# Optimization experiments

Measured on AMD Instinct MI355X. Metric: run time of the kernel, lower is better.

Reference implementation:

```python
import jax, jax.numpy as jnp
import numpy as np

B, M, D, H, K, V = 4, 2048, 1024, 16, 64, 64

def setup_inputs() -> dict:
    key = jax.random.key(0)
    ks = jax.random.split(key, 5)
    return {
        "x": jax.random.normal(ks[0], (B, M, D), dtype=jnp.float32),
        "P_q": jax.random.normal(ks[1], (H, D, K), dtype=jnp.float32) * 0.02,
        "P_k": jax.random.normal(ks[2], (H, D, K), dtype=jnp.float32) * 0.02,
        "P_v": jax.random.normal(ks[3], (H, D, V), dtype=jnp.float32) * 0.02,
        "P_o": jax.random.normal(ks[4], (H, D, V), dtype=jnp.float32) * 0.02,
    }

def reference(x, P_q, P_k, P_v, P_o):
    # QKV projections: [b,m,d] x [h,d,k] -> [b,h,m,k]
    Q = jnp.einsum('bmd,hdk->bhmk', x, P_q)
    Kt = jnp.einsum('bmd,hdk->bhmk', x, P_k)
    Vt = jnp.einsum('bmd,hdv->bhmv', x, P_v)
    scale = 1.0 / jnp.sqrt(jnp.asarray(K, dtype=x.dtype))
    logits = jnp.einsum('bhmk,bhnk->bhmn', Q, Kt) * scale  # [b,h,m,m]
    m = logits.shape[-1]
    causal = jnp.tril(jnp.ones((m, m), dtype=bool))  # allow j <= i
    logits = jnp.where(causal[None, None], logits, jnp.asarray(-jnp.inf, dtype=logits.dtype))
    weights = jax.nn.softmax(logits, axis=-1)
    o = jnp.einsum('bhmn,bhnv->bhmv', weights, Vt)
    y = jnp.einsum('bhmv,hdv->bmd', o, P_o)
    return y
```

## Files before the change

kernel.cpp:

```cpp
#include <hip/hip_runtime.h>
#include <hip/hip_bf16.h>

#define B_  4
#define M_  2048
#define D_  1024
#define H_  16

typedef __attribute__((ext_vector_type(8)))  short bf16x8;
typedef __attribute__((ext_vector_type(4)))  float f32x4;
typedef __attribute__((ext_vector_type(16))) float f32x16;
typedef __attribute__((ext_vector_type(4)))  unsigned short u16x4;
typedef __attribute__((ext_vector_type(2)))  unsigned int uint2v;

#define MFMA16(a, b, c) __builtin_amdgcn_mfma_f32_16x16x32_bf16((a), (b), (c), 0, 0, 0)
#define MFMA32(a, b, c) __builtin_amdgcn_mfma_f32_32x32x16_bf16((a), (b), (c), 0, 0, 0)

#define QSCALE 0.18033688011112042f

__device__ __forceinline__ unsigned short f2b(float f) {
  union { float f; unsigned u; } v; v.f = f;
  unsigned r = v.u + 0x7FFF + ((v.u >> 16) & 1);
  return (unsigned short)(r >> 16);
}

__device__ __forceinline__ unsigned cvtpk(float lo, float hi) {
  unsigned r;
  asm("v_cvt_pk_bf16_f32 %0, %1, %2" : "=v"(r) : "v"(lo), "v"(hi));
  return r;
}

__device__ __forceinline__ int swzb(int byte) {
  return byte ^ (((byte >> 7) & 7) << 4);
}

#define SWZ256(L) ((L) ^ ((((L) >> 8) & 15) << 4))

#define GLOAD16(gsrc, ldst)                                                     \
  __builtin_amdgcn_global_load_lds(                                             \
      (const __attribute__((address_space(1))) void*)(gsrc),                    \
      (__attribute__((address_space(3))) void*)(ldst), 16, 0, 0)

__global__ __launch_bounds__(256) void convert_x_kernel(
    const float* __restrict__ x, short* __restrict__ xb) {
  const size_t i = ((size_t)blockIdx.x * 256 + threadIdx.x) * 8;
  float4 a = *(const float4*)(x + i);
  float4 b = *(const float4*)(x + i + 4);
  bf16x8 o;
  o[0] = (short)f2b(a.x); o[1] = (short)f2b(a.y); o[2] = (short)f2b(a.z); o[3] = (short)f2b(a.w);
  o[4] = (short)f2b(b.x); o[5] = (short)f2b(b.y); o[6] = (short)f2b(b.z); o[7] = (short)f2b(b.w);
  *(bf16x8*)(xb + i) = o;
}

__global__ __launch_bounds__(256) void convert_w_kernel(
    const float* __restrict__ Pq, const float* __restrict__ Pk,
    const float* __restrict__ Pv, short* __restrict__ Wt) {
  const int idx = blockIdx.x * 256 + threadIdx.x;
  const int n = idx >> 8, d0 = (idx & 255) * 4;
  const int which = n >> 10, h = (n >> 6) & 15, kc = n & 63;
  const float* P = (which == 0) ? Pq : (which == 1) ? Pk : Pv;
  const float* p = P + ((size_t)h * D_ + d0) * 64 + kc;
  u16x4 o;
  o[0] = f2b(p[0]); o[1] = f2b(p[64]); o[2] = f2b(p[128]); o[3] = f2b(p[192]);
  *(u16x4*)(Wt + (size_t)n * D_ + d0) = o;
}

__global__ __launch_bounds__(256) void convert_wo_kernel(
    const float* __restrict__ Po, short* __restrict__ Wo) {
  const int idx = blockIdx.x * 256 + threadIdx.x;
  const int d = idx >> 8, hv0 = (idx & 255) * 4;
  const int h = hv0 >> 6, v = hv0 & 63;
  float4 a = *(const float4*)(Po + ((size_t)h * D_ + d) * 64 + v);
  u16x4 o;
  o[0] = f2b(a.x); o[1] = f2b(a.y); o[2] = f2b(a.z); o[3] = f2b(a.w);
  *(u16x4*)(Wo + (size_t)d * 1024 + hv0) = o;
}

__global__ __launch_bounds__(256) void qkv_gemm_kernel(
    const short* __restrict__ xb, const short* __restrict__ Wt,
    short* __restrict__ Qw, short* __restrict__ Kw, short* __restrict__ Vt) {
  __shared__ short As[128 * 64];
  __shared__ short Bs[128 * 64];
  int bid = blockIdx.x;
  bid = (bid & 7) * 192 + (bid >> 3);
  const int mt = bid & 63, nt = bid >> 6;
  const int m0 = mt * 128, n0 = nt * 128;
  const int t = threadIdx.x, lane = t & 63, w = t >> 6;
  const int wr = (w >> 1) * 64, wc = (w & 1) * 64;
  const int lrow = lane & 15, lgrp = lane >> 4;

  f32x4 acc[4][4] = {};
  const char* Agc = (const char*)xb + (size_t)m0 * D_ * 2;
  const char* Bgc = (const char*)Wt + (size_t)n0 * D_ * 2;

  for (int d0 = 0; d0 < D_; d0 += 64) {
    __syncthreads();
#pragma unroll
    for (int i = 0; i < 4; ++i) {
      const int L = i * 4096 + t * 16;
      const int row = L >> 7;
      const int cb = (L & 127) ^ ((row & 7) << 4);
      GLOAD16(Agc + ((size_t)row * D_ + d0) * 2 + cb, (char*)As + i * 4096 + w * 1024);
      GLOAD16(Bgc + ((size_t)row * D_ + d0) * 2 + cb, (char*)Bs + i * 4096 + w * 1024);
    }
    __syncthreads();
#pragma unroll
    for (int ks = 0; ks < 2; ++ks) {
      bf16x8 a[4], b[4];
      const int cb = ks * 64 + lgrp * 16;
#pragma unroll
      for (int f = 0; f < 4; ++f) {
        a[f] = *(const bf16x8*)((const char*)As + swzb((wr + f * 16 + lrow) * 128 + cb));
        b[f] = *(const bf16x8*)((const char*)Bs + swzb((wc + f * 16 + lrow) * 128 + cb));
      }
#pragma unroll
      for (int mf = 0; mf < 4; ++mf)
#pragma unroll
        for (int nf = 0; nf < 4; ++nf)
          acc[mf][nf] = MFMA16(a[mf], b[nf], acc[mf][nf]);
    }
  }

#pragma unroll
  for (int nf = 0; nf < 4; ++nf) {
    const int n = n0 + wc + nf * 16 + lrow;
    const int which = n >> 10, h = (n >> 6) & 15, kc = n & 63;
#pragma unroll
    for (int mf = 0; mf < 4; ++mf) {
      const int row0 = m0 + wr + mf * 16 + lgrp * 4;
      const int b = row0 >> 11, mm = row0 & 2047;
      const int bh = b * 16 + h;
      if (which == 2) {
        u16x4 o;
        o[0] = f2b(acc[mf][nf][0]); o[1] = f2b(acc[mf][nf][1]);
        o[2] = f2b(acc[mf][nf][2]); o[3] = f2b(acc[mf][nf][3]);
        *(u16x4*)(Vt + ((size_t)bh * 64 + kc) * M_ + mm) = o;
      } else {
        short* outp = (which == 0 ? Qw : Kw) + ((size_t)bh * M_ + mm) * 64 + kc;
        const float scale = (which == 0) ? QSCALE : 1.0f;
#pragma unroll
        for (int r = 0; r < 4; ++r)
          outp[(size_t)r * 64] = (short)f2b(acc[mf][nf][r] * scale);
      }
    }
  }
}

__device__ __forceinline__ void softmax_chunk(
    f32x16& s0, f32x16& s1, f32x16& o0, f32x16& o1,
    float& mrun, float& lrun, bf16x8 (&pf)[4])
{
  float tm[16];
#pragma unroll
  for (int r = 0; r < 16; ++r) tm[r] = fmaxf(s0[r], s1[r]);
#pragma unroll
  for (int st = 8; st > 0; st >>= 1)
#pragma unroll
    for (int r = 0; r < 8; ++r)
      if (r < st) tm[r] = fmaxf(tm[r], tm[r + st]);
  uint2v pm = __builtin_amdgcn_permlane32_swap(
      __float_as_uint(tm[0]), __float_as_uint(tm[0]), false, false);
  const float mtile = fmaxf(__uint_as_float(pm[0]), __uint_as_float(pm[1]));

  if (!__all(mtile <= mrun + 8.0f)) {
    const float mnew = fmaxf(mrun, mtile);
    const float alpha = __builtin_amdgcn_exp2f(mrun - mnew);
    mrun = mnew;
    lrun *= alpha;
    o0 *= alpha;
    o1 *= alpha;
  }
#pragma unroll
  for (int r = 0; r < 16; ++r) {
    s0[r] = __builtin_amdgcn_exp2f(s0[r] - mrun);
    s1[r] = __builtin_amdgcn_exp2f(s1[r] - mrun);
  }
#pragma unroll
  for (int c = 0; c < 4; ++c) {
    const f32x16& sv = (c < 2) ? s0 : s1;
    const int rb = (c & 1) * 8;
    unsigned a0 = cvtpk(sv[rb + 0], sv[rb + 1]);
    unsigned a1 = cvtpk(sv[rb + 2], sv[rb + 3]);
    unsigned b0 = cvtpk(sv[rb + 4], sv[rb + 5]);
    unsigned b1 = cvtpk(sv[rb + 6], sv[rb + 7]);
    uint2v t0 = __builtin_amdgcn_permlane32_swap(a0, b0, false, false);
    uint2v t1 = __builtin_amdgcn_permlane32_swap(a1, b1, false, false);
    union { unsigned u[4]; bf16x8 v; } pk;
    pk.u[0] = t0[0]; pk.u[1] = t1[0]; pk.u[2] = t0[1]; pk.u[3] = t1[1];
    pf[c] = pk.v;
  }
}

__global__ __launch_bounds__(256) void attn_kernel(
    const short* __restrict__ Qw, const short* __restrict__ Kw,
    const short* __restrict__ Vt, short* __restrict__ O2) {
  __shared__ short Ks[2][64 * 64];
  __shared__ short Vs[2][64 * 64];

  const int bid = blockIdx.x;
  const int chunk = 15 - (bid >> 6);
  const int bh = bid & 63;
  const int q0 = chunk * 128;

  const int t = threadIdx.x, lane = t & 63, w = t >> 6;
  const int l31 = lane & 31, hi = lane >> 5;
  const int qw0 = q0 + w * 32;
  const int qabs = qw0 + l31;

  bf16x8 qfrag[4];
#pragma unroll
  for (int kc = 0; kc < 4; ++kc)
    qfrag[kc] = *(const bf16x8*)(Qw + ((size_t)bh * M_ + qabs) * 64 + kc * 16 + hi * 8);

  f32x16 o0 = {}, o1 = {};
  float mrun = -3.0e38f, lrun = 0.f;

  const char* Kg = (const char*)Kw + (size_t)bh * M_ * 128;
  const char* Vg = (const char*)Vt + (size_t)bh * 64 * M_ * 2;

  auto stage = [&](int bi, int j0_) {
#pragma unroll
    for (int i = 0; i < 2; ++i) {
      const int L  = i * 4096 + t * 16;
      const int Ls = SWZ256(L);
      const int row = Ls >> 7, col = Ls & 127;
      GLOAD16(Kg + (size_t)(j0_ + row) * 128 + col, (char*)Ks[bi] + i * 4096 + w * 1024);
      GLOAD16(Vg + (size_t)row * (M_ * 2) + (size_t)j0_ * 2 + col, (char*)Vs[bi] + i * 4096 + w * 1024);
    }
  };

  const int nt = (q0 + 128) >> 6;
  stage(0, 0);

  bf16x8 ones;
#pragma unroll
  for (int e = 0; e < 8; ++e) ones[e] = (short)0x3F80;

  for (int tt = 0; tt < nt; ++tt) {
    const int j0 = tt << 6;
    const int cur = tt & 1;
    __builtin_amdgcn_s_barrier();
    if (tt + 1 < nt) {
      stage(cur ^ 1, j0 + 64);
      asm volatile("s_waitcnt vmcnt(4)" ::: "memory");
    } else {
      asm volatile("s_waitcnt vmcnt(0)" ::: "memory");
    }
    __builtin_amdgcn_s_barrier();
    if (j0 >= qw0 + 32) continue;

    const char* Kc = (const char*)Ks[cur];
    const char* Vc = (const char*)Vs[cur];

    f32x16 s0 = {}, s1 = {};
    __builtin_amdgcn_s_setprio(1);
#pragma unroll
    for (int kc = 0; kc < 4; ++kc) {
      bf16x8 kf0 = *(const bf16x8*)(Kc + SWZ256(l31 * 128 + kc * 32 + hi * 16));
      s0 = MFMA32(kf0, qfrag[kc], s0);
      bf16x8 kf1 = *(const bf16x8*)(Kc + SWZ256((32 + l31) * 128 + kc * 32 + hi * 16));
      s1 = MFMA32(kf1, qfrag[kc], s1);
    }
    __builtin_amdgcn_s_setprio(0);

    if (j0 + 64 > qw0) {
#pragma unroll
      for (int r = 0; r < 16; ++r) {
        const int k0 = j0 + (r & 3) + 8 * (r >> 2) + 4 * hi;
        if (k0 > qabs)      s0[r] = -3.0e38f;
        if (k0 + 32 > qabs) s1[r] = -3.0e38f;
      }
    }

    bf16x8 pf[4];
    softmax_chunk(s0, s1, o0, o1, mrun, lrun, pf);

    f32x16 lacc = {};
    __builtin_amdgcn_s_setprio(1);
#pragma unroll
    for (int c = 0; c < 4; ++c) {
      bf16x8 vf0 = *(const bf16x8*)(Vc + SWZ256(l31 * 128 + c * 32 + hi * 16));
      o0 = MFMA32(vf0, pf[c], o0);
      bf16x8 vf1 = *(const bf16x8*)(Vc + SWZ256((32 + l31) * 128 + c * 32 + hi * 16));
      o1 = MFMA32(vf1, pf[c], o1);
      lacc = MFMA32(ones, pf[c], lacc);
    }
    __builtin_amdgcn_s_setprio(0);
    lrun += lacc[0];
  }

  const int b = bh >> 4, h = bh & 15;
  const float inv = 1.0f / lrun;
  short* orow = O2 + ((size_t)b * M_ + qabs) * 1024 + h * 64;
#pragma unroll
  for (int vb = 0; vb < 2; ++vb) {
    const f32x16& o = vb ? o1 : o0;
#pragma unroll
    for (int g = 0; g < 4; ++g) {
      const int vbase = vb * 32 + 8 * g + 4 * hi;
      u16x4 pkt;
      pkt[0] = f2b(o[g * 4 + 0] * inv);
      pkt[1] = f2b(o[g * 4 + 1] * inv);
      pkt[2] = f2b(o[g * 4 + 2] * inv);
      pkt[3] = f2b(o[g * 4 + 3] * inv);
      *(u16x4*)(orow + vbase) = pkt;
    }
  }
}

__global__ __launch_bounds__(256) void out_gemm_kernel(
    const short* __restrict__ O2, const short* __restrict__ Wo,
    float* __restrict__ y) {
  __shared__ short As[128 * 64];
  __shared__ short Bs[128 * 64];
  int bid = blockIdx.x;
  bid = (bid & 7) * 64 + (bid >> 3);
  const int mt = bid & 63, nt = bid >> 6;
  const int m0 = mt * 128, n0 = nt * 128;
  const int t = threadIdx.x, lane = t & 63, w = t >> 6;
  const int wr = (w >> 1) * 64, wc = (w & 1) * 64;
  const int lrow = lane & 15, lgrp = lane >> 4;

  f32x4 acc[4][4] = {};
  const char* Agc = (const char*)O2 + (size_t)m0 * 1024 * 2;
  const char* Bgc = (const char*)Wo + (size_t)n0 * 1024 * 2;

  for (int d0 = 0; d0 < 1024; d0 += 64) {
    __syncthreads();
#pragma unroll
    for (int i = 0; i < 4; ++i) {
      const int L = i * 4096 + t * 16;
      const int row = L >> 7;
      const int cb = (L & 127) ^ ((row & 7) << 4);
      GLOAD16(Agc + ((size_t)row * 1024 + d0) * 2 + cb, (char*)As + i * 4096 + w * 1024);
      GLOAD16(Bgc + ((size_t)row * 1024 + d0) * 2 + cb, (char*)Bs + i * 4096 + w * 1024);
    }
    __syncthreads();
#pragma unroll
    for (int ks = 0; ks < 2; ++ks) {
      bf16x8 a[4], b[4];
      const int cb = ks * 64 + lgrp * 16;
#pragma unroll
      for (int f = 0; f < 4; ++f) {
        a[f] = *(const bf16x8*)((const char*)As + swzb((wr + f * 16 + lrow) * 128 + cb));
        b[f] = *(const bf16x8*)((const char*)Bs + swzb((wc + f * 16 + lrow) * 128 + cb));
      }
#pragma unroll
      for (int mf = 0; mf < 4; ++mf)
#pragma unroll
        for (int nf = 0; nf < 4; ++nf)
          acc[mf][nf] = MFMA16(a[mf], b[nf], acc[mf][nf]);
    }
  }

#pragma unroll
  for (int mf = 0; mf < 4; ++mf)
#pragma unroll
    for (int nf = 0; nf < 4; ++nf) {
      const int n = n0 + wc + nf * 16 + lrow;
      const int row0 = m0 + wr + mf * 16 + lgrp * 4;
#pragma unroll
      for (int r = 0; r < 4; ++r)
        y[(size_t)(row0 + r) * 1024 + n] = acc[mf][nf][r];
    }
}

extern "C" void kernel_launch(void* const* d_in, const int* in_sizes, int n_in,
                              void* d_out, int out_size, void* d_ws, size_t ws_size,
                              hipStream_t stream) {
  const float* x  = (const float*)d_in[0];
  const float* Pq = (const float*)d_in[1];
  const float* Pk = (const float*)d_in[2];
  const float* Pv = (const float*)d_in[3];
  const float* Po = (const float*)d_in[4];
  float* y = (float*)d_out;

  short* ws = (short*)d_ws;
  const size_t NX = (size_t)B_ * M_ * D_;
  short* xb  = ws;                 ws += NX;
  short* Wt  = ws;                 ws += (size_t)3072 * 1024;
  short* Wo  = ws;                 ws += (size_t)1024 * 1024;
  short* Qw  = ws;                 ws += NX;
  short* Kw  = ws;                 ws += NX;
  short* Vt  = ws;                 ws += NX;
  short* O2  = ws;                 ws += NX;

  convert_x_kernel <<<4096, 256, 0, stream>>>(x, xb);
  convert_w_kernel <<<3072, 256, 0, stream>>>(Pq, Pk, Pv, Wt);
  convert_wo_kernel<<<1024, 256, 0, stream>>>(Po, Wo);
  qkv_gemm_kernel  <<<1536, 256, 0, stream>>>(xb, Wt, Qw, Kw, Vt);
  attn_kernel      <<<1024, 256, 0, stream>>>(Qw, Kw, Vt, O2);
  out_gemm_kernel  <<<512,  256, 0, stream>>>(O2, Wo, y);
}
```

Measured before the change: 200.3 us.

## Double-buffer GEMM K-tiles with 128x256 blocks and 8 waves

Both projection GEMMs now share one body that uses 128x256 output tiles with 512 threads and a K-step of 128. The K-tiles are double-buffered in LDS: the next tile's global-to-LDS loads are issued before computing the current one, with partial vmcnt waits. MFMA bursts run at raised wave priority, and blocks are mapped to XCDs so that neighbouring M tiles share a chip. The aim is to hide global load latency and raise reuse per block. In exchange the kernel uses 96KB of LDS per block, which limits occupancy, and launches fewer blocks.

Measured after the change: 188.6 us. -5.9%, faster.

```diff
diff --git a/kernel.cpp b/kernel.cpp
--- a/kernel.cpp
+++ b/kernel.cpp
@@ -75,58 +75,92 @@
   *(u16x4*)(Wo + (size_t)d * 1024 + hv0) = o;
 }
 
-__global__ __launch_bounds__(256) void qkv_gemm_kernel(
-    const short* __restrict__ xb, const short* __restrict__ Wt,
-    short* __restrict__ Qw, short* __restrict__ Kw, short* __restrict__ Vt) {
-  __shared__ short As[128 * 64];
-  __shared__ short Bs[128 * 64];
-  int bid = blockIdx.x;
-  bid = (bid & 7) * 192 + (bid >> 3);
-  const int mt = bid & 63, nt = bid >> 6;
-  const int m0 = mt * 128, n0 = nt * 128;
-  const int t = threadIdx.x, lane = t & 63, w = t >> 6;
-  const int wr = (w >> 1) * 64, wc = (w & 1) * 64;
+__device__ __forceinline__ void gemm_body_128x256(
+    const char* __restrict__ Agc, const char* __restrict__ Bgc,
+    short* AsBase, short* BsBase, int t, int w, int lane,
+    f32x4 (&acc)[4][4])
+{
+  const int wm = w >> 2, wn = w & 3;
   const int lrow = lane & 15, lgrp = lane >> 4;
 
-  f32x4 acc[4][4] = {};
-  const char* Agc = (const char*)xb + (size_t)m0 * D_ * 2;
-  const char* Bgc = (const char*)Wt + (size_t)n0 * D_ * 2;
-
-  for (int d0 = 0; d0 < D_; d0 += 64) {
-    __syncthreads();
+  auto stage = [&](int bi, int kt) {
+    const int d2 = kt * 128;
+#pragma unroll
+    for (int i = 0; i < 2; ++i) {
+      const int L = i * 8192 + t * 16;
+      const int row = L >> 7;
+      const int cs = (L & 127) ^ ((row & 7) << 4);
+      GLOAD16(Agc + (size_t)row * 2048 + d2 + cs, (char*)AsBase + bi * 16384 + L);
+    }
 #pragma unroll
     for (int i = 0; i < 4; ++i) {
-      const int L = i * 4096 + t * 16;
+      const int L = i * 8192 + t * 16;
       const int row = L >> 7;
-      const int cb = (L & 127) ^ ((row & 7) << 4);
-      GLOAD16(Agc + ((size_t)row * D_ + d0) * 2 + cb, (char*)As + i * 4096 + w * 1024);
-      GLOAD16(Bgc + ((size_t)row * D_ + d0) * 2 + cb, (char*)Bs + i * 4096 + w * 1024);
-    }
-    __syncthreads();
+      const int cs = (L & 127) ^ ((row & 7) << 4);
+      GLOAD16(Bgc + (size_t)row * 2048 + d2 + cs, (char*)BsBase + bi * 32768 + L);
+    }
+  };
+
+  stage(0, 0);
+
+  for (int kt = 0; kt < 16; ++kt) {
+    const int cur = kt & 1;
+    __builtin_amdgcn_s_barrier();
+    if (kt + 1 < 16) {
+      stage(cur ^ 1, kt + 1);
+      asm volatile("s_waitcnt vmcnt(6)" ::: "memory");
+    } else {
+      asm volatile("s_waitcnt vmcnt(0)" ::: "memory");
+    }
+    __builtin_amdgcn_s_barrier();
+
+    const char* Ac = (const char*)AsBase + cur * 16384;
+    const char* Bc = (const char*)BsBase + cur * 32768;
 #pragma unroll
     for (int ks = 0; ks < 2; ++ks) {
       bf16x8 a[4], b[4];
       const int cb = ks * 64 + lgrp * 16;
 #pragma unroll
       for (int f = 0; f < 4; ++f) {
-        a[f] = *(const bf16x8*)((const char*)As + swzb((wr + f * 16 + lrow) * 128 + cb));
-        b[f] = *(const bf16x8*)((const char*)Bs + swzb((wc + f * 16 + lrow) * 128 + cb));
+        a[f] = *(const bf16x8*)(Ac + swzb((wm * 64 + f * 16 + lrow) * 128 + cb));
+        b[f] = *(const bf16x8*)(Bc + swzb((wn * 64 + f * 16 + lrow) * 128 + cb));
       }
+      __builtin_amdgcn_s_setprio(1);
 #pragma unroll
       for (int mf = 0; mf < 4; ++mf)
 #pragma unroll
         for (int nf = 0; nf < 4; ++nf)
           acc[mf][nf] = MFMA16(a[mf], b[nf], acc[mf][nf]);
-    }
-  }
-
+      __builtin_amdgcn_s_setprio(0);
+    }
+  }
+}
+
+__global__ __launch_bounds__(512) void qkv_gemm_kernel(
+    const short* __restrict__ xb, const short* __restrict__ Wt,
+    short* __restrict__ Qw, short* __restrict__ Kw, short* __restrict__ Vt) {
+  __shared__ short As[2][8192];
+  __shared__ short Bs[2][16384];
+  const int bid = blockIdx.x;
+  const int xcd = bid & 7, slot = bid >> 3;
+  const int m0 = (xcd * 8 + (slot & 7)) * 128;
+  const int n0 = (slot >> 3) * 256;
+  const int t = threadIdx.x, lane = t & 63, w = t >> 6;
+
+  f32x4 acc[4][4] = {};
+  gemm_body_128x256((const char*)xb + (size_t)m0 * 2048,
+                    (const char*)Wt + (size_t)n0 * 2048,
+                    &As[0][0], &Bs[0][0], t, w, lane, acc);
+
+  const int wm = w >> 2, wn = w & 3;
+  const int lrow = lane & 15, lgrp = lane >> 4;
 #pragma unroll
   for (int nf = 0; nf < 4; ++nf) {
-    const int n = n0 + wc + nf * 16 + lrow;
+    const int n = n0 + wn * 64 + nf * 16 + lrow;
     const int which = n >> 10, h = (n >> 6) & 15, kc = n & 63;
 #pragma unroll
     for (int mf = 0; mf < 4; ++mf) {
-      const int row0 = m0 + wr + mf * 16 + lgrp * 4;
+      const int row0 = m0 + wm * 64 + mf * 16 + lgrp * 4;
       const int b = row0 >> 11, mm = row0 & 2047;
       const int bh = b * 16 + h;
       if (which == 2) {
@@ -143,6 +177,36 @@
       }
     }
   }
+}
+
+__global__ __launch_bounds__(512) void out_gemm_kernel(
+    const short* __restrict__ O2, const short* __restrict__ Wo,
+    float* __restrict__ y) {
+  __shared__ short As[2][8192];
+  __shared__ short Bs[2][16384];
+  const int bid = blockIdx.x;
+  const int xcd = bid & 7, slot = bid >> 3;
+  const int m0 = (xcd * 8 + (slot & 7)) * 128;
+  const int n0 = (slot >> 3) * 256;
+  const int t = threadIdx.x, lane = t & 63, w = t >> 6;
+
+  f32x4 acc[4][4] = {};
+  gemm_body_128x256((const char*)O2 + (size_t)m0 * 2048,
+                    (const char*)Wo + (size_t)n0 * 2048,
+                    &As[0][0], &Bs[0][0], t, w, lane, acc);
+
+  const int wm = w >> 2, wn = w & 3;
+  const int lrow = lane & 15, lgrp = lane >> 4;
+#pragma unroll
+  for (int mf = 0; mf < 4; ++mf)
+#pragma unroll
+    for (int nf = 0; nf < 4; ++nf) {
+      const int n = n0 + wn * 64 + nf * 16 + lrow;
+      const int row0 = m0 + wm * 64 + mf * 16 + lgrp * 4;
+#pragma unroll
+      for (int r = 0; r < 4; ++r)
+        y[(size_t)(row0 + r) * 1024 + n] = acc[mf][nf][r];
+    }
 }
 
 __device__ __forceinline__ void softmax_chunk(
@@ -307,63 +371,6 @@
   }
 }
 
-__global__ __launch_bounds__(256) void out_gemm_kernel(
-    const short* __restrict__ O2, const short* __restrict__ Wo,
-    float* __restrict__ y) {
-  __shared__ short As[128 * 64];
-  __shared__ short Bs[128 * 64];
-  int bid = blockIdx.x;
-  bid = (bid & 7) * 64 + (bid >> 3);
-  const int mt = bid & 63, nt = bid >> 6;
-  const int m0 = mt * 128, n0 = nt * 128;
-  const int t = threadIdx.x, lane = t & 63, w = t >> 6;
-  const int wr = (w >> 1) * 64, wc = (w & 1) * 64;
-  const int lrow = lane & 15, lgrp = lane >> 4;
-
-  f32x4 acc[4][4] = {};
-  const char* Agc = (const char*)O2 + (size_t)m0 * 1024 * 2;
-  const char* Bgc = (const char*)Wo + (size_t)n0 * 1024 * 2;
-
-  for (int d0 = 0; d0 < 1024; d0 += 64) {
-    __syncthreads();
-#pragma unroll
-    for (int i = 0; i < 4; ++i) {
-      const int L = i * 4096 + t * 16;
-      const int row = L >> 7;
-      const int cb = (L & 127) ^ ((row & 7) << 4);
-      GLOAD16(Agc + ((size_t)row * 1024 + d0) * 2 + cb, (char*)As + i * 4096 + w * 1024);
-      GLOAD16(Bgc + ((size_t)row * 1024 + d0) * 2 + cb, (char*)Bs + i * 4096 + w * 1024);
-    }
-    __syncthreads();
-#pragma unroll
-    for (int ks = 0; ks < 2; ++ks) {
-      bf16x8 a[4], b[4];
-      const int cb = ks * 64 + lgrp * 16;
-#pragma unroll
-      for (int f = 0; f < 4; ++f) {
-        a[f] = *(const bf16x8*)((const char*)As + swzb((wr + f * 16 + lrow) * 128 + cb));
-        b[f] = *(const bf16x8*)((const char*)Bs + swzb((wc + f * 16 + lrow) * 128 + cb));
-      }
-#pragma unroll
-      for (int mf = 0; mf < 4; ++mf)
-#pragma unroll
-        for (int nf = 0; nf < 4; ++nf)
-          acc[mf][nf] = MFMA16(a[mf], b[nf], acc[mf][nf]);
-    }
-  }
-
-#pragma unroll
-  for (int mf = 0; mf < 4; ++mf)
-#pragma unroll
-    for (int nf = 0; nf < 4; ++nf) {
-      const int n = n0 + wc + nf * 16 + lrow;
-      const int row0 = m0 + wr + mf * 16 + lgrp * 4;
-#pragma unroll
-      for (int r = 0; r < 4; ++r)
-        y[(size_t)(row0 + r) * 1024 + n] = acc[mf][nf][r];
-    }
-}
-
 extern "C" void kernel_launch(void* const* d_in, const int* in_sizes, int n_in,
                               void* d_out, int out_size, void* d_ws, size_t ws_size,
                               hipStream_t stream) {
@@ -387,7 +394,7 @@
   convert_x_kernel <<<4096, 256, 0, stream>>>(x, xb);
   convert_w_kernel <<<3072, 256, 0, stream>>>(Pq, Pk, Pv, Wt);
   convert_wo_kernel<<<1024, 256, 0, stream>>>(Po, Wo);
-  qkv_gemm_kernel  <<<1536, 256, 0, stream>>>(xb, Wt, Qw, Kw, Vt);
+  qkv_gemm_kernel  <<<768,  512, 0, stream>>>(xb, Wt, Qw, Kw, Vt);
   attn_kernel      <<<1024, 256, 0, stream>>>(Qw, Kw, Vt, O2);
-  out_gemm_kernel  <<<512,  256, 0, stream>>>(O2, Wo, y);
-}
+  out_gemm_kernel  <<<256,  512, 0, stream>>>(O2, Wo, y);
+}
```
